# Kernel optimization log

Hardware: AMD Instinct MI355X
Metric: run time of the kernel (lower is better)

The kernel has to match this reference:

```python
import jax, jax.numpy as jnp
import numpy as np
from jax import lax

B, C, F, T = 32, 1, 128, 8000
FLOOR = 1e-06


def setup_inputs() -> dict:
    key = jax.random.key(0)
    mag_spec = jax.random.uniform(key, (B, C, F, T), dtype=jnp.float32)  # non-negative magnitudes
    alpha = jnp.full((C,), 0.96, dtype=jnp.float32)
    delta = jnp.full((C,), 2.0, dtype=jnp.float32)
    root = jnp.full((C,), 2.0, dtype=jnp.float32)
    smooth = jnp.full((1,), 0.04, dtype=jnp.float32)  # per_channel_smoothing=False -> shape (1,)
    return {"mag_spec": mag_spec, "alpha": alpha, "delta": delta, "root": root, "smooth": smooth}


def reference(mag_spec, alpha, delta, root, smooth):
    # mag_spec: [B, C, F, T]
    w = jnp.clip(smooth, 0.0, 1.0)[:, None]          # broadcast over (C, F) per time-step
    xs = jnp.moveaxis(mag_spec, -1, 0)               # [T, B, C, F]
    init = xs[0]                                     # initial_state = mag_spec[..., 0]

    def step(acc, x):
        acc = w * x + (1.0 - w) * acc
        return acc, acc

    final, ema = lax.scan(step, init, xs)            # ema: [T, B, C, F]
    ema = jnp.moveaxis(ema, 0, -1)                   # [B, C, F, T]

    a = jnp.minimum(alpha, 1.0)[:, None, None]       # (C,1,1) -> broadcast over F,T
    d = delta[:, None, None]
    one_over_root = 1.0 / jnp.maximum(root, 1.0)[:, None, None]

    out = (mag_spec / (FLOOR + ema) ** a + d) ** one_over_root - d ** one_over_root
    hidden_state = final[..., None]                  # [B, C, F, 1]
    return out, hidden_state
```

## Files before the change

kernel.cpp:

```cpp
#include <hip/hip_runtime.h>

#define FLOOR_EPS 1e-6f

constexpr int Bq = 32, Cq = 1, Fq = 128, Tq = 8000;
constexpr int ROWS = Bq * Cq * Fq;
constexpr int LPR  = 8;
constexpr int RNDE = 64 * LPR;
constexpr int NR   = (Tq + RNDE - 1) / RNDE;
constexpr int LACT = (Tq - (NR - 1) * RNDE) / LPR;
constexpr int WPB  = 4;

__global__ __launch_bounds__(256, 4)
void _PCEN_75033078661345_kernel(const float* __restrict__ x,
                                 const float* __restrict__ alpha,
                                 const float* __restrict__ delta,
                                 const float* __restrict__ root,
                                 const float* __restrict__ smooth,
                                 float* __restrict__ out,
                                 float* __restrict__ hid)
{
    const int lane = threadIdx.x & 63;
    const int wid  = threadIdx.x >> 6;
    const int r    = blockIdx.x * WPB + wid;
    const int c    = (r / Fq) % Cq;

    const float w   = fminf(fmaxf(smooth[0], 0.f), 1.f);
    const float om  = 1.f - w;
    const float aa  = fminf(alpha[c], 1.f);
    const float dd  = delta[c];
    const float oor = 1.f / fmaxf(root[c], 1.f);
    const bool  us  = (oor == 0.5f);
    const float droot = us ? __builtin_amdgcn_sqrtf(dd)
                           : __builtin_amdgcn_exp2f(oor * __builtin_amdgcn_logf(dd));

    float om2 = om * om, om4 = om2 * om2;
    float omp[6];
    omp[0] = om4 * om4;
    #pragma unroll
    for (int k = 1; k < 6; ++k) omp[k] = omp[k - 1] * omp[k - 1];
    float om8i = 1.f;
    #pragma unroll
    for (int k = 0; k < 6; ++k) om8i = ((lane >> k) & 1) ? om8i * omp[k] : om8i;
    const float omR = omp[5] * omp[5];

    const float* row  = x   + (size_t)r * Tq;
    float*       orow = out + (size_t)r * Tq;

    float carry = row[0];

    float4 buf[3][2];
    #pragma unroll
    for (int s = 0; s < 2; ++s) {
        const float4* p = (const float4*)(row + s * RNDE + lane * LPR);
        buf[s][0] = p[0]; buf[s][1] = p[1];
    }

    float accL = 0.f;
    #pragma unroll
    for (int s = 0; s < NR; ++s) {
        if (s + 2 < NR) {
            const bool pact = (s + 2 < NR - 1) || (lane < LACT);
            float4 n0 = {0,0,0,0}, n1 = {0,0,0,0};
            if (pact) {
                const float4* p = (const float4*)(row + (s + 2) * RNDE + lane * LPR);
                n0 = p[0]; n1 = p[1];
            }
            buf[(s + 2) % 3][0] = n0; buf[(s + 2) % 3][1] = n1;
        }

        const float4 c0 = buf[s % 3][0], c1 = buf[s % 3][1];
        const float xv[LPR] = {c0.x, c0.y, c0.z, c0.w, c1.x, c1.y, c1.z, c1.w};

        float b = 0.f;
        #pragma unroll
        for (int j = 0; j < LPR; ++j) b = w * xv[j] + om * b;

        #pragma unroll
        for (int k = 0; k < 6; ++k) {
            const float pb = __shfl_up(b, 1 << k);
            const float nb = fmaf(omp[k], pb, b);
            b = (lane >= (1 << k)) ? nb : b;
        }
        const float pb1 = __shfl_up(b, 1);
        const float bex = (lane == 0) ? 0.f : pb1;
        float acc = fmaf(om8i, carry, bex);
        const float btot = __shfl(b, 63);
        carry = fmaf(omR, carry, btot);

        float ov[LPR];
        #pragma unroll
        for (int j = 0; j < LPR; ++j) {
            acc = w * xv[j] + om * acc;
            const float dp = __builtin_amdgcn_exp2f(-aa * __builtin_amdgcn_logf(FLOOR_EPS + acc));
            const float tt = fmaf(xv[j], dp, dd);
            ov[j] = us ? (__builtin_amdgcn_sqrtf(tt) - droot)
                       : (__builtin_amdgcn_exp2f(oor * __builtin_amdgcn_logf(tt)) - droot);
        }
        const bool act = (s < NR - 1) || (lane < LACT);
        if (act) {
            float4* q = (float4*)(orow + s * RNDE + lane * LPR);
            float4 o0 = {ov[0], ov[1], ov[2], ov[3]};
            float4 o1 = {ov[4], ov[5], ov[6], ov[7]};
            q[0] = o0; q[1] = o1;
        }
        accL = acc;
    }

    const float h = __shfl(accL, LACT - 1);
    if (lane == 0) hid[r] = h;
}

extern "C" void kernel_launch(void* const* d_in, const int* in_sizes, int n_in,
                              void* d_out, int out_size, void* d_ws, size_t ws_size,
                              hipStream_t stream) {
    const float* x      = (const float*)d_in[0];
    const float* alpha  = (const float*)d_in[1];
    const float* delta  = (const float*)d_in[2];
    const float* root   = (const float*)d_in[3];
    const float* smooth = (const float*)d_in[4];
    float* out = (float*)d_out;
    float* hid = out + (size_t)ROWS * Tq;

    _PCEN_75033078661345_kernel<<<ROWS / WPB, 256, 0, stream>>>(
        x, alpha, delta, root, smooth, out, hid);
}
```

Baseline: 63.09 us.

## Split each row's scan across two wavefronts using a decaying warm-up window

Each row is now handled by two wavefronts. The second half starts a few rounds early and runs a warm-up scan over the preceding data, relying on the exponential decay of (1-w) so the inherited state becomes negligible. This doubles the wavefront count to improve latency hiding and occupancy on a sequential scan that is bound by memory latency. The cost is redundant loads and scan work for the warm-up region, plus an approximation of the recurrence whose accuracy depends on the smoothing coefficient. The loop is no longer fully unrolled and the launch-bounds occupancy hint was removed.

```diff
diff --git a/kernel.cpp b/kernel.cpp
--- a/kernel.cpp
+++ b/kernel.cpp
@@ -3,14 +3,17 @@
 #define FLOOR_EPS 1e-6f
 
 constexpr int Bq = 32, Cq = 1, Fq = 128, Tq = 8000;
-constexpr int ROWS = Bq * Cq * Fq;
-constexpr int LPR  = 8;
-constexpr int RNDE = 64 * LPR;
-constexpr int NR   = (Tq + RNDE - 1) / RNDE;
-constexpr int LACT = (Tq - (NR - 1) * RNDE) / LPR;
-constexpr int WPB  = 4;
+constexpr int ROWS  = Bq * Cq * Fq;
+constexpr int LPR   = 8;
+constexpr int RNDE  = 64 * LPR;
+constexpr int SPLIT = 2;
+constexpr int MAIN  = Tq / SPLIT;
+constexpr int NRM   = (MAIN + RNDE - 1) / RNDE;
+constexpr int LACT  = (MAIN - (NRM - 1) * RNDE) / LPR;
+constexpr int WPB   = 4;
+constexpr unsigned TOTE = (unsigned)ROWS * Tq;
 
-__global__ __launch_bounds__(256, 4)
+__global__ __launch_bounds__(256)
 void _PCEN_75033078661345_kernel(const float* __restrict__ x,
                                  const float* __restrict__ alpha,
                                  const float* __restrict__ delta,
@@ -21,7 +24,9 @@
 {
     const int lane = threadIdx.x & 63;
     const int wid  = threadIdx.x >> 6;
-    const int r    = blockIdx.x * WPB + wid;
+    const int gw   = blockIdx.x * WPB + wid;
+    const int r    = gw >> 1;
+    const int h    = gw & 1;
     const int c    = (r / Fq) % Cq;
 
     const float w   = fminf(fmaxf(smooth[0], 0.f), 1.f);
@@ -43,71 +48,81 @@
     for (int k = 0; k < 6; ++k) om8i = ((lane >> k) & 1) ? om8i * omp[k] : om8i;
     const float omR = omp[5] * omp[5];
 
-    const float* row  = x   + (size_t)r * Tq;
-    float*       orow = out + (size_t)r * Tq;
+    int Rw = 0;
+    if (h) {
+        const float nl2 = fmaxf(-__builtin_amdgcn_logf(om), 1e-9f);
+        float need = 30.f / (512.f * nl2);
+        int ri = (int)ceilf(need);
+        Rw = ri < 1 ? 1 : (ri > 7 ? 7 : ri);
+    }
+    const int w0 = h * MAIN - Rw * RNDE;
+    const int nr = NRM + Rw;
 
-    float carry = row[0];
+    const unsigned rowbase = (unsigned)r * (unsigned)Tq;
 
-    float4 buf[3][2];
-    #pragma unroll
-    for (int s = 0; s < 2; ++s) {
-        const float4* p = (const float4*)(row + s * RNDE + lane * LPR);
-        buf[s][0] = p[0]; buf[s][1] = p[1];
-    }
+    float carry = x[rowbase + (unsigned)w0];
+    float accv  = 0.f;
 
-    float accL = 0.f;
-    #pragma unroll
-    for (int s = 0; s < NR; ++s) {
-        if (s + 2 < NR) {
-            const bool pact = (s + 2 < NR - 1) || (lane < LACT);
-            float4 n0 = {0,0,0,0}, n1 = {0,0,0,0};
-            if (pact) {
-                const float4* p = (const float4*)(row + (s + 2) * RNDE + lane * LPR);
-                n0 = p[0]; n1 = p[1];
-            }
-            buf[(s + 2) % 3][0] = n0; buf[(s + 2) % 3][1] = n1;
-        }
+    auto LOADR = [&](int sidx, float4& d0, float4& d1) {
+        unsigned u = rowbase + (unsigned)(w0 + sidx * RNDE + lane * LPR);
+        u = u > (TOTE - LPR) ? (TOTE - LPR) : u;
+        const float4* p = (const float4*)(x + u);
+        d0 = p[0]; d1 = p[1];
+    };
 
-        const float4 c0 = buf[s % 3][0], c1 = buf[s % 3][1];
+    auto ROUND = [&](int sidx, float4 c0, float4 c1) {
         const float xv[LPR] = {c0.x, c0.y, c0.z, c0.w, c1.x, c1.y, c1.z, c1.w};
-
         float b = 0.f;
         #pragma unroll
         for (int j = 0; j < LPR; ++j) b = w * xv[j] + om * b;
-
         #pragma unroll
         for (int k = 0; k < 6; ++k) {
             const float pb = __shfl_up(b, 1 << k);
             const float nb = fmaf(omp[k], pb, b);
             b = (lane >= (1 << k)) ? nb : b;
         }
-        const float pb1 = __shfl_up(b, 1);
-        const float bex = (lane == 0) ? 0.f : pb1;
-        float acc = fmaf(om8i, carry, bex);
+        const float pb1  = __shfl_up(b, 1);
+        const float bex  = (lane == 0) ? 0.f : pb1;
+        float acc        = fmaf(om8i, carry, bex);
         const float btot = __shfl(b, 63);
         carry = fmaf(omR, carry, btot);
+        if (sidx >= Rw) {
+            float ov[LPR];
+            #pragma unroll
+            for (int j = 0; j < LPR; ++j) {
+                acc = w * xv[j] + om * acc;
+                const float dp = __builtin_amdgcn_exp2f(-aa * __builtin_amdgcn_logf(FLOOR_EPS + acc));
+                const float tt = fmaf(xv[j], dp, dd);
+                ov[j] = us ? (__builtin_amdgcn_sqrtf(tt) - droot)
+                           : (__builtin_amdgcn_exp2f(oor * __builtin_amdgcn_logf(tt)) - droot);
+            }
+            const bool lastr = (sidx == nr - 1);
+            if (!lastr || lane < LACT) {
+                float4* q = (float4*)(out + rowbase + (unsigned)(w0 + sidx * RNDE + lane * LPR));
+                float4 o0 = {ov[0], ov[1], ov[2], ov[3]};
+                float4 o1 = {ov[4], ov[5], ov[6], ov[7]};
+                q[0] = o0; q[1] = o1;
+            }
+            accv = acc;
+        }
+    };
 
-        float ov[LPR];
-        #pragma unroll
-        for (int j = 0; j < LPR; ++j) {
-            acc = w * xv[j] + om * acc;
-            const float dp = __builtin_amdgcn_exp2f(-aa * __builtin_amdgcn_logf(FLOOR_EPS + acc));
-            const float tt = fmaf(xv[j], dp, dd);
-            ov[j] = us ? (__builtin_amdgcn_sqrtf(tt) - droot)
-                       : (__builtin_amdgcn_exp2f(oor * __builtin_amdgcn_logf(tt)) - droot);
-        }
-        const bool act = (s < NR - 1) || (lane < LACT);
-        if (act) {
-            float4* q = (float4*)(orow + s * RNDE + lane * LPR);
-            float4 o0 = {ov[0], ov[1], ov[2], ov[3]};
-            float4 o1 = {ov[4], ov[5], ov[6], ov[7]};
-            q[0] = o0; q[1] = o1;
-        }
-        accL = acc;
+    float4 A0, A1, B0, B1;
+    LOADR(0, A0, A1);
+    LOADR(1, B0, B1);
+    int s = 0;
+    for (; s + 1 < nr; s += 2) {
+        float4 c0 = A0, c1 = A1;
+        if (s + 2 < nr) LOADR(s + 2, A0, A1);
+        ROUND(s, c0, c1);
+        c0 = B0; c1 = B1;
+        if (s + 3 < nr) LOADR(s + 3, B0, B1);
+        ROUND(s + 1, c0, c1);
     }
+    if (s < nr) ROUND(s, A0, A1);
 
-    const float h = __shfl(accL, LACT - 1);
-    if (lane == 0) hid[r] = h;
+    const float hh = __shfl(accv, LACT - 1);
+    if (h == 1 && lane == 0) hid[r] = hh;
 }
 
 extern "C" void kernel_launch(void* const* d_in, const int* in_sizes, int n_in,
@@ -121,6 +136,6 @@
     float* out = (float*)d_out;
     float* hid = out + (size_t)ROWS * Tq;
 
-    _PCEN_75033078661345_kernel<<<ROWS / WPB, 256, 0, stream>>>(
+    _PCEN_75033078661345_kernel<<<(ROWS * SPLIT) / WPB, 256, 0, stream>>>(
         x, alpha, delta, root, smooth, out, hid);
 }
```

New measurement: 53.26 us. 1.18x faster.
